# Kernel tuning notes

Measured on AMD Instinct MI355X. Metric: run time of the kernel, lower is better.

Reference implementation:

```python
import jax, jax.numpy as jnp
import numpy as np

TREE_DEPTH = 10
TOTAL = 2 ** (TREE_DEPTH + 1) - 1  # 2047 nodes per tree
G = 64                              # graphs per batch
N = G * TOTAL                       # 131008 nodes
E = 2 * N                           # 262016 directed edges
H = 256                             # h_dim
HALF = H // 2
L = 4                               # num_layers
LABELS = 32
OUT = 32
BN_EPS = 1e-5
LN_EPS = 1e-5


def setup_inputs() -> dict:
    key = jax.random.key(0)
    ks = jax.random.split(key, 16)
    x = jnp.stack([jax.random.randint(ks[0], (N,), 0, TOTAL),
                   jax.random.randint(ks[1], (N,), 0, LABELS)], axis=1)
    edge_src = jax.random.randint(ks[2], (E,), 0, N)
    edge_dst = jax.random.randint(ks[3], (E,), 0, N)
    edge_weight = jax.random.uniform(ks[4], (E,), dtype=jnp.float32)
    batch = jnp.arange(N, dtype=jnp.int64) // TOTAL          # node -> graph id
    root_index = jnp.arange(G, dtype=jnp.int64) * TOTAL      # one root per graph
    s = 0.02
    emb_node = jax.random.normal(ks[5], (TOTAL, HALF), dtype=jnp.float32) * s
    emb_label = jax.random.normal(ks[6], (LABELS, HALF), dtype=jnp.float32) * s
    w = 1.0 / np.sqrt(H)
    W1 = jax.random.normal(ks[7], (L, H, H), dtype=jnp.float32) * w
    b1 = jnp.zeros((L, H), dtype=jnp.float32)
    g1 = jnp.ones((L, H), dtype=jnp.float32)
    be1 = jnp.zeros((L, H), dtype=jnp.float32)
    W2 = jax.random.normal(ks[8], (L, H, H), dtype=jnp.float32) * w
    b2 = jnp.zeros((L, H), dtype=jnp.float32)
    g2 = jnp.ones((L, H), dtype=jnp.float32)
    be2 = jnp.zeros((L, H), dtype=jnp.float32)
    ln_g = jnp.ones((L, H), dtype=jnp.float32)
    ln_b = jnp.zeros((L, H), dtype=jnp.float32)
    Wout = jax.random.normal(ks[9], (OUT, H), dtype=jnp.float32) * w
    return {"x": x, "edge_src": edge_src, "edge_dst": edge_dst,
            "edge_weight": edge_weight, "batch": batch, "root_index": root_index,
            "emb_node": emb_node, "emb_label": emb_label,
            "W1": W1, "b1": b1, "g1": g1, "be1": be1,
            "W2": W2, "b2": b2, "g2": g2, "be2": be2,
            "ln_g": ln_g, "ln_b": ln_b, "Wout": Wout}


def _batchnorm(h, g, b):
    # BatchNorm1d, training-mode batch statistics over the node dim
    m = h.mean(axis=0)
    v = h.var(axis=0)
    return g * (h - m) * jax.lax.rsqrt(v + BN_EPS) + b


def _layernorm(h, g, b):
    m = h.mean(axis=-1, keepdims=True)
    v = h.var(axis=-1, keepdims=True)
    return g * (h - m) * jax.lax.rsqrt(v + LN_EPS) + b


def reference(x, edge_src, edge_dst, edge_weight, batch, root_index,
              emb_node, emb_label, W1, b1, g1, be1, W2, b2, g2, be2,
              ln_g, ln_b, Wout):
    # BiEmbedding_cat: concat of two h/2 embeddings
    h = jnp.concatenate([emb_node[x[:, 0]], emb_label[x[:, 1]]], axis=-1)  # [N,H]
    target_roots = root_index[batch]  # all-nodes->root targets for last layer
    for i in range(L):
        if i == L - 1:  # last_layer_fully_adjacent: every node sends to its root
            agg = jnp.zeros_like(h).at[target_roots].add(h)
        else:
            agg = jnp.zeros_like(h).at[edge_dst].add(h[edge_src] * edge_weight[:, None])
        m = h + agg  # GIN with eps=0: (1+eps)*x + sum_j w_ij x_j
        m = jax.nn.relu(_batchnorm(m @ W1[i].T + b1[i], g1[i], be1[i]))
        m = jax.nn.relu(_batchnorm(m @ W2[i].T + b2[i], g2[i], be2[i]))
        # use_activation: relu (idempotent after the MLP's trailing relu)
        h = h + m  # use_residual
        h = _layernorm(h, ln_g[i], ln_b[i])
    roots_x = h[root_index]  # [G,H] root readout
    return roots_x @ Wout.T  # [G,OUT], bias-free out layer
```

## Files before the change

### kernel.cpp

```cpp
#include <hip/hip_runtime.h>
#include <stdint.h>

#define NN 131008
#define NPAD 131072
#define EE 262016
#define HD 256
#define GG 64
#define TT 2047

typedef __attribute__((ext_vector_type(8))) short bfrag;
typedef __attribute__((ext_vector_type(4))) float f32x4;

__device__ __forceinline__ float bflo(unsigned u){ union{unsigned i; float f;} v; v.i = u<<16; return v.f; }
__device__ __forceinline__ float bfhi(unsigned u){ union{unsigned i; float f;} v; v.i = u & 0xffff0000u; return v.f; }
__device__ __forceinline__ unsigned short f2bf(float f){
  union{unsigned i; float fl;} v; v.fl = f; unsigned i = v.i;
  return (unsigned short)((i + 0x7fffu + ((i>>16)&1u)) >> 16);
}
__device__ __forceinline__ unsigned pack2(float a, float b){
  return (unsigned)f2bf(a) | ((unsigned)f2bf(b)<<16);
}
__device__ __forceinline__ void gload16(const void* g, void* s){
  __builtin_amdgcn_global_load_lds((__attribute__((address_space(1))) void*)g,
                                   (__attribute__((address_space(3))) void*)s, 16, 0, 0);
}

__device__ __forceinline__ short bnrelu1(short t, float a, float c){
  union{unsigned i; float f;} v; v.i = ((unsigned)(unsigned short)t) << 16;
  return (short)f2bf(fmaxf(a*v.f + c, 0.f));
}
__device__ __forceinline__ bfrag bn8(bfrag t, float4 a0, float4 a1, float4 c0, float4 c1){
  bfrag r;
  r[0]=bnrelu1(t[0],a0.x,c0.x); r[1]=bnrelu1(t[1],a0.y,c0.y);
  r[2]=bnrelu1(t[2],a0.z,c0.z); r[3]=bnrelu1(t[3],a0.w,c0.w);
  r[4]=bnrelu1(t[4],a1.x,c1.x); r[5]=bnrelu1(t[5],a1.y,c1.y);
  r[6]=bnrelu1(t[6],a1.z,c1.z); r[7]=bnrelu1(t[7],a1.w,c1.w);
  return r;
}

__device__ __forceinline__ void atomic_add_bf16x2(unsigned short* p, float a, float b){
#if __has_builtin(__builtin_amdgcn_global_atomic_fadd_v2bf16)
  typedef __attribute__((ext_vector_type(2))) short s16x2;
  s16x2 v; v.x = (short)f2bf(a); v.y = (short)f2bf(b);
  __builtin_amdgcn_global_atomic_fadd_v2bf16((__attribute__((address_space(1))) s16x2*)p, v);
#else
  unsigned* up = (unsigned*)p;
  unsigned old = *up, assumed;
  do {
    assumed = old;
    unsigned nv = pack2(bflo(assumed) + a, bfhi(assumed) + b);
    old = atomicCAS(up, assumed, nv);
  } while (old != assumed);
#endif
}

__global__ void k_prep(const float* __restrict__ W1, const float* __restrict__ W2,
                       unsigned short* __restrict__ wbf,
                       const int* __restrict__ x, const float* __restrict__ en,
                       const float* __restrict__ el, unsigned short* __restrict__ hbf,
                       const int* __restrict__ ed, int* __restrict__ deg){
  int b = blockIdx.x;
  if (b < 2048){
    int idx = b*256 + threadIdx.x;
    float v = (idx < 262144) ? W1[idx] : W2[idx - 262144];
    wbf[idx] = f2bf(v);
  } else if (b < 18432){
    size_t i8 = ((size_t)(b - 2048)*256 + threadIdx.x) << 3;
    int row = (int)(i8 >> 8); int k = (int)(i8 & 255);
    uint4 o;
    if (row < NN){
      const float* src = (k < 128) ? en + (size_t)x[2*row]*128 + k
                                   : el + (size_t)x[2*row+1]*128 + (k-128);
      float4 v0 = *(const float4*)src;
      float4 v1 = *(const float4*)(src + 4);
      o.x = pack2(v0.x, v0.y); o.y = pack2(v0.z, v0.w);
      o.z = pack2(v1.x, v1.y); o.w = pack2(v1.z, v1.w);
    } else { o.x = o.y = o.z = o.w = 0u; }
    *(uint4*)(hbf + i8) = o;
  } else {
    int e = (b - 18432)*256 + threadIdx.x;
    if (e < EE) atomicAdd(&deg[ed[e]], 1);
  }
}

__global__ void k_scan_block(const int* __restrict__ deg, int* __restrict__ start,
                             int* __restrict__ bsum){
  __shared__ int sh[256];
  int t = threadIdx.x;
  int i = blockIdx.x*256 + t;
  int v = deg[i];
  int val = v; sh[t] = val; __syncthreads();
  for (int off = 1; off < 256; off <<= 1){
    int add = (t >= off) ? sh[t-off] : 0;
    __syncthreads();
    val += add; sh[t] = val;
    __syncthreads();
  }
  start[i] = val - v;
  if (t == 255) bsum[blockIdx.x] = val;
}
__global__ void k_scan_top(int* __restrict__ bsum){
  __shared__ int sh[512];
  int t = threadIdx.x;
  int v = bsum[t];
  int val = v; sh[t] = val; __syncthreads();
  for (int off = 1; off < 512; off <<= 1){
    int add = (t >= off) ? sh[t-off] : 0;
    __syncthreads();
    val += add; sh[t] = val;
    __syncthreads();
  }
  bsum[t] = val - v;
}
__global__ void k_fill(const int* __restrict__ es, const int* __restrict__ ed,
                       const float* __restrict__ ew, const int* __restrict__ start,
                       const int* __restrict__ bsum,
                       int* __restrict__ cursor0, uint2* __restrict__ pairs){
  int e = blockIdx.x*256 + threadIdx.x;
  if (e < EE){
    int d = ed[e];
    int pos = start[d] + bsum[d >> 8] + atomicAdd(&cursor0[d], 1);
    uint2 p; p.x = (unsigned)es[e];
    union{float f; unsigned u;} w; w.f = ew[e];
    p.y = w.u;
    pairs[pos] = p;
  }
}

__global__ void k_gather(const int* __restrict__ deg, const int* __restrict__ start,
                         const int* __restrict__ bsum,
                         const uint2* __restrict__ pairs,
                         const unsigned short* __restrict__ hbf,
                         unsigned short* __restrict__ mbf){
  int half = threadIdx.x >> 5, lane32 = threadIdx.x & 31;
  int row = blockIdx.x*8 + half;
  size_t base = (size_t)row*HD + (lane32 << 3);
  uint4 o;
  if (row < NN){
    uint4 hv = *(const uint4*)(hbf + base);
    float a0 = bflo(hv.x), a1 = bfhi(hv.x), a2 = bflo(hv.y), a3 = bfhi(hv.y);
    float a4 = bflo(hv.z), a5 = bfhi(hv.z), a6 = bflo(hv.w), a7 = bfhi(hv.w);
    int d = deg[row], s = start[row] + bsum[row >> 8];
    for (int j = 0; j < d; ++j){
      uint2 pr = pairs[s + j];
      union{unsigned u; float f;} wg; wg.u = pr.y;
      uint4 sv = *(const uint4*)(hbf + (size_t)pr.x*HD + (lane32 << 3));
      a0 += bflo(sv.x)*wg.f; a1 += bfhi(sv.x)*wg.f;
      a2 += bflo(sv.y)*wg.f; a3 += bfhi(sv.y)*wg.f;
      a4 += bflo(sv.z)*wg.f; a5 += bfhi(sv.z)*wg.f;
      a6 += bflo(sv.w)*wg.f; a7 += bfhi(sv.w)*wg.f;
    }
    o.x = pack2(a0, a1); o.y = pack2(a2, a3);
    o.z = pack2(a4, a5); o.w = pack2(a6, a7);
  } else { o.x = o.y = o.z = o.w = 0u; }
  *(uint4*)(mbf + base) = o;
}

__global__ void k_rootsum(const unsigned short* __restrict__ hbf, unsigned short* __restrict__ m){
  int g = blockIdx.x >> 4, ch = blockIdx.x & 15;
  int col = threadIdx.x * 2;
  int nr = (ch == 15) ? 127 : 128;
  const unsigned short* p = hbf + ((size_t)g*TT + ch*128)*HD + col;
  float a = 0.f, b = 0.f;
  for (int r = 0; r < nr; ++r){
    unsigned u = *(const unsigned*)(p + (size_t)r*HD);
    a += bflo(u); b += bfhi(u);
  }
  atomic_add_bf16x2(m + (size_t)g*TT*HD + col, a, b);
}

__global__ __launch_bounds__(512) void k_gemm(const unsigned short* __restrict__ A,
                                              const unsigned short* __restrict__ B,
                                              unsigned short* __restrict__ C,
                                              float* __restrict__ gsum, float* __restrict__ gsq){
  __shared__ unsigned short As[128*64];
  __shared__ unsigned short Bs[256*64];
  __shared__ float rs[256];
  __shared__ float rq[256];
  const int tid = threadIdx.x, lane = tid & 63, w = tid >> 6;
  const int wr = w >> 2, wc = w & 3;
  const int mb = blockIdx.x;
  if (tid < 256){ rs[tid] = 0.f; rq[tid] = 0.f; }
  f32x4 acc[4][4];
  f32x4 zz = {0.f, 0.f, 0.f, 0.f};
#pragma unroll
  for (int a = 0; a < 4; ++a)
#pragma unroll
    for (int b = 0; b < 4; ++b) acc[a][b] = zz;

  for (int kt = 0; kt < 4; ++kt){
    __syncthreads();
#pragma unroll
    for (int it = 0; it < 2; ++it){
      int ci = it*512 + tid;
      int row = ci >> 3, cp = ci & 7;
      int cl = cp ^ (row & 7);
      gload16(A + ((size_t)mb*128 + row)*HD + kt*64 + cl*8, &As[ci*8]);
    }
#pragma unroll
    for (int it = 0; it < 4; ++it){
      int ci = it*512 + tid;
      int row = ci >> 3, cp = ci & 7;
      int cl = cp ^ (row & 7);
      gload16(B + (size_t)row*HD + kt*64 + cl*8, &Bs[ci*8]);
    }
    __syncthreads();
    bfrag af[4][2], bfv[4][2];
    {
      const int q = lane >> 4, r15 = lane & 15, r7 = lane & 7;
#pragma unroll
      for (int rt = 0; rt < 4; ++rt){
        int ra = wr*64 + rt*16 + r15;
        int rb = wc*64 + rt*16 + r15;
#pragma unroll
        for (int hf = 0; hf < 2; ++hf){
          af[rt][hf]  = *(const bfrag*)&As[ra*64 + (((q + 4*hf) ^ r7) << 3)];
          bfv[rt][hf] = *(const bfrag*)&Bs[rb*64 + (((q + 4*hf) ^ r7) << 3)];
        }
      }
    }
#pragma unroll
    for (int hf = 0; hf < 2; ++hf)
#pragma unroll
      for (int rt = 0; rt < 4; ++rt)
#pragma unroll
        for (int ct = 0; ct < 4; ++ct)
          acc[rt][ct] = __builtin_amdgcn_mfma_f32_16x16x32_bf16(af[rt][hf], bfv[ct][hf], acc[rt][ct], 0, 0, 0);
  }

  const int lr0 = wr*64 + (lane >> 4)*4;
  const int lc0 = wc*64 + (lane & 15);
  float cs[4] = {0.f,0.f,0.f,0.f}, cq[4] = {0.f,0.f,0.f,0.f};
#pragma unroll
  for (int rt = 0; rt < 4; ++rt){
#pragma unroll
    for (int ct = 0; ct < 4; ++ct){
#pragma unroll
      for (int i = 0; i < 4; ++i){
        size_t grow = (size_t)mb*128 + lr0 + rt*16 + i;
        float v = acc[rt][ct][i];
        C[grow*HD + lc0 + ct*16] = f2bf(v);
        if (grow < NN){ cs[ct] += v; cq[ct] += v*v; }
      }
    }
  }
#pragma unroll
  for (int ct = 0; ct < 4; ++ct){
    float s = cs[ct], q = cq[ct];
    s += __shfl_xor(s, 16); s += __shfl_xor(s, 32);
    q += __shfl_xor(q, 16); q += __shfl_xor(q, 32);
    if ((lane >> 4) == 0){
      atomicAdd(&rs[lc0 + ct*16], s);
      atomicAdd(&rq[lc0 + ct*16], q);
    }
  }
  __syncthreads();
  if (tid < 256){
    atomicAdd(&gsum[tid], rs[tid]);
    atomicAdd(&gsq[tid], rq[tid]);
  }
}

__global__ __launch_bounds__(512) void k_gemm2(const unsigned short* __restrict__ T,
                                               const float* __restrict__ sum1,
                                               const float* __restrict__ sq1,
                                               const float* __restrict__ g1v,
                                               const float* __restrict__ be1v,
                                               const unsigned short* __restrict__ B,
                                               unsigned short* __restrict__ C,
                                               float* __restrict__ gsum, float* __restrict__ gsq){
  __shared__ unsigned short As[128*64];
  __shared__ unsigned short Bs[256*64];
  __shared__ float rs[256];
  __shared__ float rq[256];
  __shared__ float acf[256];
  __shared__ float ccf[256];
  const int tid = threadIdx.x, lane = tid & 63, w = tid >> 6;
  const int wr = w >> 2, wc = w & 3;
  const int mb = blockIdx.x;
  if (tid < 256){
    rs[tid] = 0.f; rq[tid] = 0.f;
    const float inv_n = 1.f/(float)NN;
    float mean = sum1[tid] * inv_n;
    float var  = fmaxf(sq1[tid] * inv_n - mean*mean, 0.f);
    float aj   = g1v[tid] * rsqrtf(var + 1e-5f);
    acf[tid] = aj;
    ccf[tid] = be1v[tid] - aj*mean;
  }
  f32x4 acc[4][4];
  f32x4 zz = {0.f, 0.f, 0.f, 0.f};
#pragma unroll
  for (int a = 0; a < 4; ++a)
#pragma unroll
    for (int b = 0; b < 4; ++b) acc[a][b] = zz;

  for (int kt = 0; kt < 4; ++kt){
    __syncthreads();
#pragma unroll
    for (int it = 0; it < 2; ++it){
      int ci = it*512 + tid;
      int row = ci >> 3, cp = ci & 7;
      int cl = cp ^ (row & 7);
      gload16(T + ((size_t)mb*128 + row)*HD + kt*64 + cl*8, &As[ci*8]);
    }
#pragma unroll
    for (int it = 0; it < 4; ++it){
      int ci = it*512 + tid;
      int row = ci >> 3, cp = ci & 7;
      int cl = cp ^ (row & 7);
      gload16(B + (size_t)row*HD + kt*64 + cl*8, &Bs[ci*8]);
    }
    asm volatile("s_waitcnt vmcnt(4)" ::: "memory");
#pragma unroll
    for (int it = 0; it < 2; ++it){
      int ci = it*512 + tid;
      int row = ci >> 3, cp = ci & 7;
      int kb = (cp ^ (row & 7)) << 3;
      bfrag v = *(const bfrag*)&As[ci*8];
      float4 a0 = *(const float4*)&acf[kt*64 + kb];
      float4 a1 = *(const float4*)&acf[kt*64 + kb + 4];
      float4 c0 = *(const float4*)&ccf[kt*64 + kb];
      float4 c1 = *(const float4*)&ccf[kt*64 + kb + 4];
      *(bfrag*)&As[ci*8] = bn8(v, a0, a1, c0, c1);
    }
    __syncthreads();
    bfrag af[4][2], bfv[4][2];
    {
      const int q = lane >> 4, r15 = lane & 15, r7 = lane & 7;
#pragma unroll
      for (int rt = 0; rt < 4; ++rt){
        int ra = wr*64 + rt*16 + r15;
        int rb = wc*64 + rt*16 + r15;
#pragma unroll
        for (int hf = 0; hf < 2; ++hf){
          af[rt][hf]  = *(const bfrag*)&As[ra*64 + (((q + 4*hf) ^ r7) << 3)];
          bfv[rt][hf] = *(const bfrag*)&Bs[rb*64 + (((q + 4*hf) ^ r7) << 3)];
        }
      }
    }
#pragma unroll
    for (int hf = 0; hf < 2; ++hf)
#pragma unroll
      for (int rt = 0; rt < 4; ++rt)
#pragma unroll
        for (int ct = 0; ct < 4; ++ct)
          acc[rt][ct] = __builtin_amdgcn_mfma_f32_16x16x32_bf16(af[rt][hf], bfv[ct][hf], acc[rt][ct], 0, 0, 0);
  }

  const int lr0 = wr*64 + (lane >> 4)*4;
  const int lc0 = wc*64 + (lane & 15);
  float cs[4] = {0.f,0.f,0.f,0.f}, cq[4] = {0.f,0.f,0.f,0.f};
#pragma unroll
  for (int rt = 0; rt < 4; ++rt){
#pragma unroll
    for (int ct = 0; ct < 4; ++ct){
#pragma unroll
      for (int i = 0; i < 4; ++i){
        size_t grow = (size_t)mb*128 + lr0 + rt*16 + i;
        float v = acc[rt][ct][i];
        C[grow*HD + lc0 + ct*16] = f2bf(v);
        if (grow < NN){ cs[ct] += v; cq[ct] += v*v; }
      }
    }
  }
#pragma unroll
  for (int ct = 0; ct < 4; ++ct){
    float s = cs[ct], q = cq[ct];
    s += __shfl_xor(s, 16); s += __shfl_xor(s, 32);
    q += __shfl_xor(q, 16); q += __shfl_xor(q, 32);
    if ((lane >> 4) == 0){
      atomicAdd(&rs[lc0 + ct*16], s);
      atomicAdd(&rq[lc0 + ct*16], q);
    }
  }
  __syncthreads();
  if (tid < 256){
    atomicAdd(&gsum[tid], rs[tid]);
    atomicAdd(&gsq[tid], rq[tid]);
  }
}

__device__ __forceinline__ void coef4(float4 s4, float4 q4, float4 g4, float4 b4,
                                      float4& a, float4& c){
  const float inv_n = 1.f/(float)NN;
  float m0 = s4.x*inv_n, m1 = s4.y*inv_n, m2 = s4.z*inv_n, m3 = s4.w*inv_n;
  float i0 = rsqrtf(fmaxf(q4.x*inv_n - m0*m0, 0.f) + 1e-5f);
  float i1 = rsqrtf(fmaxf(q4.y*inv_n - m1*m1, 0.f) + 1e-5f);
  float i2 = rsqrtf(fmaxf(q4.z*inv_n - m2*m2, 0.f) + 1e-5f);
  float i3 = rsqrtf(fmaxf(q4.w*inv_n - m3*m3, 0.f) + 1e-5f);
  a.x = g4.x*i0; a.y = g4.y*i1; a.z = g4.z*i2; a.w = g4.w*i3;
  c.x = b4.x - a.x*m0; c.y = b4.y - a.y*m1; c.z = b4.z - a.z*m2; c.w = b4.w - a.w*m3;
}

__global__ void k_fuse(const unsigned short* t2,
                       const float* __restrict__ sum, const float* __restrict__ sq,
                       const float* __restrict__ g, const float* __restrict__ be,
                       const float* __restrict__ lg, const float* __restrict__ lb,
                       unsigned short* __restrict__ hbf, unsigned short* mbf,
                       int writem){
  int half = threadIdx.x >> 5, lane32 = threadIdx.x & 31;
  size_t row = (size_t)blockIdx.x*8 + half;
  int col = lane32 << 3;
  size_t base = row*HD + col;
  uint4 o;
  if (row < NN){
    float4 av0, cv0, av1, cv1;
    coef4(*(const float4*)(sum + col),     *(const float4*)(sq + col),
          *(const float4*)(g + col),       *(const float4*)(be + col),     av0, cv0);
    coef4(*(const float4*)(sum + col + 4), *(const float4*)(sq + col + 4),
          *(const float4*)(g + col + 4),   *(const float4*)(be + col + 4), av1, cv1);
    uint4 tv = *(const uint4*)(t2 + base);
    uint4 hv = *(const uint4*)(hbf + base);
    float r0 = bflo(hv.x) + fmaxf(av0.x*bflo(tv.x) + cv0.x, 0.f);
    float r1 = bfhi(hv.x) + fmaxf(av0.y*bfhi(tv.x) + cv0.y, 0.f);
    float r2 = bflo(hv.y) + fmaxf(av0.z*bflo(tv.y) + cv0.z, 0.f);
    float r3 = bfhi(hv.y) + fmaxf(av0.w*bfhi(tv.y) + cv0.w, 0.f);
    float r4 = bflo(hv.z) + fmaxf(av1.x*bflo(tv.z) + cv1.x, 0.f);
    float r5 = bfhi(hv.z) + fmaxf(av1.y*bfhi(tv.z) + cv1.y, 0.f);
    float r6 = bflo(hv.w) + fmaxf(av1.z*bflo(tv.w) + cv1.z, 0.f);
    float r7 = bfhi(hv.w) + fmaxf(av1.w*bfhi(tv.w) + cv1.w, 0.f);
    float s  = r0+r1+r2+r3+r4+r5+r6+r7;
    float qq = r0*r0+r1*r1+r2*r2+r3*r3+r4*r4+r5*r5+r6*r6+r7*r7;
#pragma unroll
    for (int d = 1; d < 32; d <<= 1){ s += __shfl_xor(s, d); qq += __shfl_xor(qq, d); }
    float mean = s * (1.f/256.f);
    float var  = fmaxf(qq * (1.f/256.f) - mean*mean, 0.f);
    float inv  = rsqrtf(var + 1e-5f);
    float4 gv0 = *(const float4*)(lg + col), gv1 = *(const float4*)(lg + col + 4);
    float4 bv0 = *(const float4*)(lb + col), bv1 = *(const float4*)(lb + col + 4);
    o.x = pack2(gv0.x*(r0 - mean)*inv + bv0.x, gv0.y*(r1 - mean)*inv + bv0.y);
    o.y = pack2(gv0.z*(r2 - mean)*inv + bv0.z, gv0.w*(r3 - mean)*inv + bv0.w);
    o.z = pack2(gv1.x*(r4 - mean)*inv + bv1.x, gv1.y*(r5 - mean)*inv + bv1.y);
    o.w = pack2(gv1.z*(r6 - mean)*inv + bv1.z, gv1.w*(r7 - mean)*inv + bv1.w);
  } else {
    o.x = o.y = o.z = o.w = 0u;
  }
  *(uint4*)(hbf + base) = o;
  if (writem) *(uint4*)(mbf + base) = o;
}

__global__ void k_readout(const unsigned short* __restrict__ hbf, const float* __restrict__ Wo,
                          float* __restrict__ out){
  int g = blockIdx.x;
  int w = threadIdx.x >> 6, lane = threadIdx.x & 63;
  uint2 hv = *(const uint2*)(hbf + (size_t)g*TT*HD + (lane<<2));
  float h0 = bflo(hv.x), h1 = bfhi(hv.x), h2 = bflo(hv.y), h3 = bfhi(hv.y);
#pragma unroll
  for (int oo = 0; oo < 8; ++oo){
    int o = w*8 + oo;
    float4 wv = *(const float4*)(Wo + (size_t)o*HD + (lane<<2));
    float p = h0*wv.x + h1*wv.y + h2*wv.z + h3*wv.w;
#pragma unroll
    for (int d = 1; d < 64; d <<= 1) p += __shfl_xor(p, d);
    if (lane == 0) out[g*32 + o] = p;
  }
}

extern "C" void kernel_launch(void* const* d_in, const int* in_sizes, int n_in,
                              void* d_out, int out_size, void* d_ws, size_t ws_size,
                              hipStream_t stream){
  const int*   x   = (const int*)d_in[0];
  const int*   es  = (const int*)d_in[1];
  const int*   ed  = (const int*)d_in[2];
  const float* ew  = (const float*)d_in[3];
  const float* en  = (const float*)d_in[6];
  const float* el  = (const float*)d_in[7];
  const float* W1  = (const float*)d_in[8];
  const float* g1  = (const float*)d_in[10];
  const float* be1 = (const float*)d_in[11];
  const float* W2  = (const float*)d_in[12];
  const float* g2  = (const float*)d_in[14];
  const float* be2 = (const float*)d_in[15];
  const float* lg  = (const float*)d_in[16];
  const float* lb  = (const float*)d_in[17];
  const float* Wo  = (const float*)d_in[18];

  char* ws = (char*)d_ws;
  unsigned short* hbf = (unsigned short*)ws;
  unsigned short* mbf = (unsigned short*)(ws + 67108864);
  unsigned short* t   = (unsigned short*)(ws + 134217728);
  unsigned short* wbf = (unsigned short*)(ws + 201326592);
  float* stats   = (float*)(ws + 202375168);
  int*   deg     = (int*)  (ws + 202391552);
  int*   cursor0 = (int*)  (ws + 202915840);
  int*   start   = (int*)  (ws + 203440128);
  int*   bsum    = (int*)  (ws + 203964416);
  uint2* pairs   = (uint2*)(ws + 203968512);

  hipMemsetAsync(stats, 0, 16384 + 524288 + 524288, stream);
  k_prep<<<19456, 256, 0, stream>>>(W1, W2, wbf, x, en, el, hbf, ed, deg);

  k_scan_block<<<512, 256, 0, stream>>>(deg, start, bsum);
  k_scan_top  <<<1,   512, 0, stream>>>(bsum);
  k_fill      <<<1024,256, 0, stream>>>(es, ed, ew, start, bsum, cursor0, pairs);

  for (int i = 0; i < 4; ++i){
    float* s1 = stats + (2*i)*512;
    float* s2 = stats + (2*i+1)*512;
    if (i < 3) k_gather <<<16384, 256, 0, stream>>>(deg, start, bsum, pairs, hbf, mbf);
    else       k_rootsum<<<1024,  128, 0, stream>>>(hbf, mbf);

    k_gemm <<<1024, 512, 0, stream>>>(mbf, wbf + i*65536, t, s1, s1 + 256);
    k_gemm2<<<1024, 512, 0, stream>>>(t, s1, s1 + 256, g1 + i*256, be1 + i*256,
                                      wbf + 262144 + i*65536, mbf, s2, s2 + 256);
    k_fuse <<<16384, 256, 0, stream>>>(mbf, s2, s2 + 256, g2 + i*256, be2 + i*256,
                                       lg + i*256, lb + i*256, hbf, mbf, (i == 2) ? 1 : 0);
  }

  k_readout<<<64, 256, 0, stream>>>(hbf, Wo, (float*)d_out);
  (void)in_sizes; (void)n_in; (void)out_size; (void)ws_size;
}
```

Measured before the change: 865.4 us.

## Make GEMMs persistent with resident weights and triple-buffered A pipeline

Both node-MLP GEMM kernels now share a templated body where each block loads the full 256x256 bf16 weight matrix into LDS once and then processes four 128-row tiles. A is streamed in 32-wide K slices through a three-slot buffer with async loads two stages ahead. The grid shrinks from 1024 to 256 blocks to amortise weight loading and BN-stat reduction. The cost is about 150KB of LDS per block, which limits occupancy to one block per CU and leaves 256 blocks on 256 CUs with no spare parallelism; the per-slice barriers also add synchronisation.

```diff
diff --git a/kernel.cpp b/kernel.cpp
--- a/kernel.cpp
+++ b/kernel.cpp
@@ -169,98 +169,153 @@
   atomic_add_bf16x2(m + (size_t)g*TT*HD + col, a, b);
 }
 
+template<bool TRANS>
+__device__ __forceinline__ void gemm_body(const unsigned short* __restrict__ A,
+                                          const unsigned short* __restrict__ B,
+                                          unsigned short* __restrict__ C,
+                                          float* __restrict__ gsum, float* __restrict__ gsq,
+                                          const float* __restrict__ sum1,
+                                          const float* __restrict__ sq1,
+                                          const float* __restrict__ g1v,
+                                          const float* __restrict__ be1v){
+  __shared__ unsigned short Bs[65536];
+  __shared__ unsigned short Ar[3*4096];
+  __shared__ float acf[256];
+  __shared__ float ccf[256];
+  const int tid = threadIdx.x, lane = tid & 63, w = tid >> 6;
+  const int wr = w >> 2, wc = w & 3;
+  const int b = blockIdx.x;
+  const int q = lane >> 4, r15 = lane & 15, r7 = lane & 7;
+  const int NTS = 32;
+
+  if (TRANS && tid < 256){
+    const float inv_n = 1.f/(float)NN;
+    float mean = sum1[tid] * inv_n;
+    float var  = fmaxf(sq1[tid] * inv_n - mean*mean, 0.f);
+    float aj   = g1v[tid] * rsqrtf(var + 1e-5f);
+    acf[tid] = aj;
+    ccf[tid] = be1v[tid] - aj*mean;
+  }
+
+#pragma unroll
+  for (int kt = 0; kt < 4; ++kt)
+#pragma unroll
+    for (int it = 0; it < 4; ++it){
+      int ci = it*512 + tid;
+      int row = ci >> 3, cp = ci & 7;
+      int cl = cp ^ (row & 7);
+      gload16(B + (size_t)row*HD + kt*64 + cl*8, &Bs[kt*16384 + ci*8]);
+    }
+  {
+    const int row = tid >> 2, cp = tid & 3;
+    gload16(A + ((size_t)(b*4)*128 + row)*HD + 0*32 + cp*8, &Ar[0*4096 + tid*8]);
+    gload16(A + ((size_t)(b*4)*128 + row)*HD + 1*32 + cp*8, &Ar[1*4096 + tid*8]);
+  }
+
+  f32x4 acc[4][4];
+  f32x4 zz = {0.f, 0.f, 0.f, 0.f};
+#pragma unroll
+  for (int a = 0; a < 4; ++a)
+#pragma unroll
+    for (int c = 0; c < 4; ++c) acc[a][c] = zz;
+  float cs[4] = {0.f,0.f,0.f,0.f}, cq[4] = {0.f,0.f,0.f,0.f};
+
+  for (int s = 0; s < NTS; ++s){
+    const int slot = s % 3;
+    if (s == NTS-1) asm volatile("s_waitcnt vmcnt(0)" ::: "memory");
+    else            asm volatile("s_waitcnt vmcnt(1)" ::: "memory");
+    asm volatile("s_waitcnt lgkmcnt(0)" ::: "memory");
+    __builtin_amdgcn_s_barrier();
+    __builtin_amdgcn_sched_barrier(0);
+
+    if (s + 2 < NTS){
+      const int c = s + 2;
+      const int tile2 = b*4 + (c >> 3), ks2 = c & 7;
+      const int row = tid >> 2, cp = tid & 3;
+      gload16(A + ((size_t)tile2*128 + row)*HD + ks2*32 + cp*8,
+              &Ar[(c % 3)*4096 + tid*8]);
+    }
+
+    if (TRANS){
+      const int ks = s & 7;
+      const int kb = ks*32 + (tid & 3)*8;
+      bfrag v = *(const bfrag*)&Ar[slot*4096 + tid*8];
+      float4 a0 = *(const float4*)&acf[kb];
+      float4 a1 = *(const float4*)&acf[kb + 4];
+      float4 c0 = *(const float4*)&ccf[kb];
+      float4 c1 = *(const float4*)&ccf[kb + 4];
+      *(bfrag*)&Ar[slot*4096 + tid*8] = bn8(v, a0, a1, c0, c1);
+      asm volatile("s_waitcnt lgkmcnt(0)" ::: "memory");
+      __builtin_amdgcn_s_barrier();
+      __builtin_amdgcn_sched_barrier(0);
+    }
+
+    const int kt64 = (s >> 1) & 3, hf = s & 1;
+    bfrag af[4], bf[4];
+#pragma unroll
+    for (int rt = 0; rt < 4; ++rt){
+      int ra = wr*64 + rt*16 + r15;
+      af[rt] = *(const bfrag*)&Ar[slot*4096 + ra*32 + (q << 3)];
+    }
+#pragma unroll
+    for (int ct = 0; ct < 4; ++ct){
+      int rb = wc*64 + ct*16 + r15;
+      bf[ct] = *(const bfrag*)&Bs[kt64*16384 + rb*64 + (((q + 4*hf) ^ r7) << 3)];
+    }
+#pragma unroll
+    for (int rt = 0; rt < 4; ++rt)
+#pragma unroll
+      for (int ct = 0; ct < 4; ++ct)
+        acc[rt][ct] = __builtin_amdgcn_mfma_f32_16x16x32_bf16(af[rt], bf[ct], acc[rt][ct], 0, 0, 0);
+
+    if ((s & 7) == 7){
+      const int tile = b*4 + (s >> 3);
+      const int lr0 = wr*64 + q*4;
+      const int lc0 = wc*64 + r15;
+#pragma unroll
+      for (int rt = 0; rt < 4; ++rt)
+#pragma unroll
+        for (int ct = 0; ct < 4; ++ct){
+#pragma unroll
+          for (int i = 0; i < 4; ++i){
+            size_t grow = (size_t)tile*128 + lr0 + rt*16 + i;
+            float v = acc[rt][ct][i];
+            C[grow*HD + lc0 + ct*16] = f2bf(v);
+            if (grow < NN){ cs[ct] += v; cq[ct] += v*v; }
+          }
+          acc[rt][ct] = zz;
+        }
+    }
+  }
+
+  __syncthreads();
+  float* st = (float*)Ar;
+  st[tid < 512 ? tid : 0] = 0.f;
+  __syncthreads();
+  const int lc0 = wc*64 + r15;
+#pragma unroll
+  for (int ct = 0; ct < 4; ++ct){
+    float s2 = cs[ct], q2 = cq[ct];
+    s2 += __shfl_xor(s2, 16); s2 += __shfl_xor(s2, 32);
+    q2 += __shfl_xor(q2, 16); q2 += __shfl_xor(q2, 32);
+    if (q == 0){
+      atomicAdd(&st[lc0 + ct*16], s2);
+      atomicAdd(&st[256 + lc0 + ct*16], q2);
+    }
+  }
+  __syncthreads();
+  if (tid < 256){
+    atomicAdd(&gsum[tid], st[tid]);
+    atomicAdd(&gsq[tid], st[256 + tid]);
+  }
+}
+
 __global__ __launch_bounds__(512) void k_gemm(const unsigned short* __restrict__ A,
                                               const unsigned short* __restrict__ B,
                                               unsigned short* __restrict__ C,
                                               float* __restrict__ gsum, float* __restrict__ gsq){
-  __shared__ unsigned short As[128*64];
-  __shared__ unsigned short Bs[256*64];
-  __shared__ float rs[256];
-  __shared__ float rq[256];
-  const int tid = threadIdx.x, lane = tid & 63, w = tid >> 6;
-  const int wr = w >> 2, wc = w & 3;
-  const int mb = blockIdx.x;
-  if (tid < 256){ rs[tid] = 0.f; rq[tid] = 0.f; }
-  f32x4 acc[4][4];
-  f32x4 zz = {0.f, 0.f, 0.f, 0.f};
-#pragma unroll
-  for (int a = 0; a < 4; ++a)
-#pragma unroll
-    for (int b = 0; b < 4; ++b) acc[a][b] = zz;
-
-  for (int kt = 0; kt < 4; ++kt){
-    __syncthreads();
-#pragma unroll
-    for (int it = 0; it < 2; ++it){
-      int ci = it*512 + tid;
-      int row = ci >> 3, cp = ci & 7;
-      int cl = cp ^ (row & 7);
-      gload16(A + ((size_t)mb*128 + row)*HD + kt*64 + cl*8, &As[ci*8]);
-    }
-#pragma unroll
-    for (int it = 0; it < 4; ++it){
-      int ci = it*512 + tid;
-      int row = ci >> 3, cp = ci & 7;
-      int cl = cp ^ (row & 7);
-      gload16(B + (size_t)row*HD + kt*64 + cl*8, &Bs[ci*8]);
-    }
-    __syncthreads();
-    bfrag af[4][2], bfv[4][2];
-    {
-      const int q = lane >> 4, r15 = lane & 15, r7 = lane & 7;
-#pragma unroll
-      for (int rt = 0; rt < 4; ++rt){
-        int ra = wr*64 + rt*16 + r15;
-        int rb = wc*64 + rt*16 + r15;
-#pragma unroll
-        for (int hf = 0; hf < 2; ++hf){
-          af[rt][hf]  = *(const bfrag*)&As[ra*64 + (((q + 4*hf) ^ r7) << 3)];
-          bfv[rt][hf] = *(const bfrag*)&Bs[rb*64 + (((q + 4*hf) ^ r7) << 3)];
-        }
-      }
-    }
-#pragma unroll
-    for (int hf = 0; hf < 2; ++hf)
-#pragma unroll
-      for (int rt = 0; rt < 4; ++rt)
-#pragma unroll
-        for (int ct = 0; ct < 4; ++ct)
-          acc[rt][ct] = __builtin_amdgcn_mfma_f32_16x16x32_bf16(af[rt][hf], bfv[ct][hf], acc[rt][ct], 0, 0, 0);
-  }
-
-  const int lr0 = wr*64 + (lane >> 4)*4;
-  const int lc0 = wc*64 + (lane & 15);
-  float cs[4] = {0.f,0.f,0.f,0.f}, cq[4] = {0.f,0.f,0.f,0.f};
-#pragma unroll
-  for (int rt = 0; rt < 4; ++rt){
-#pragma unroll
-    for (int ct = 0; ct < 4; ++ct){
-#pragma unroll
-      for (int i = 0; i < 4; ++i){
-        size_t grow = (size_t)mb*128 + lr0 + rt*16 + i;
-        float v = acc[rt][ct][i];
-        C[grow*HD + lc0 + ct*16] = f2bf(v);
-        if (grow < NN){ cs[ct] += v; cq[ct] += v*v; }
-      }
-    }
-  }
-#pragma unroll
-  for (int ct = 0; ct < 4; ++ct){
-    float s = cs[ct], q = cq[ct];
-    s += __shfl_xor(s, 16); s += __shfl_xor(s, 32);
-    q += __shfl_xor(q, 16); q += __shfl_xor(q, 32);
-    if ((lane >> 4) == 0){
-      atomicAdd(&rs[lc0 + ct*16], s);
-      atomicAdd(&rq[lc0 + ct*16], q);
-    }
-  }
-  __syncthreads();
-  if (tid < 256){
-    atomicAdd(&gsum[tid], rs[tid]);
-    atomicAdd(&gsq[tid], rq[tid]);
-  }
-}
-
+  gemm_body<false>(A, B, C, gsum, gsq, nullptr, nullptr, nullptr, nullptr);
+}
 __global__ __launch_bounds__(512) void k_gemm2(const unsigned short* __restrict__ T,
                                                const float* __restrict__ sum1,
                                                const float* __restrict__ sq1,
@@ -269,115 +324,7 @@
                                                const unsigned short* __restrict__ B,
                                                unsigned short* __restrict__ C,
                                                float* __restrict__ gsum, float* __restrict__ gsq){
-  __shared__ unsigned short As[128*64];
-  __shared__ unsigned short Bs[256*64];
-  __shared__ float rs[256];
-  __shared__ float rq[256];
-  __shared__ float acf[256];
-  __shared__ float ccf[256];
-  const int tid = threadIdx.x, lane = tid & 63, w = tid >> 6;
-  const int wr = w >> 2, wc = w & 3;
-  const int mb = blockIdx.x;
-  if (tid < 256){
-    rs[tid] = 0.f; rq[tid] = 0.f;
-    const float inv_n = 1.f/(float)NN;
-    float mean = sum1[tid] * inv_n;
-    float var  = fmaxf(sq1[tid] * inv_n - mean*mean, 0.f);
-    float aj   = g1v[tid] * rsqrtf(var + 1e-5f);
-    acf[tid] = aj;
-    ccf[tid] = be1v[tid] - aj*mean;
-  }
-  f32x4 acc[4][4];
-  f32x4 zz = {0.f, 0.f, 0.f, 0.f};
-#pragma unroll
-  for (int a = 0; a < 4; ++a)
-#pragma unroll
-    for (int b = 0; b < 4; ++b) acc[a][b] = zz;
-
-  for (int kt = 0; kt < 4; ++kt){
-    __syncthreads();
-#pragma unroll
-    for (int it = 0; it < 2; ++it){
-      int ci = it*512 + tid;
-      int row = ci >> 3, cp = ci & 7;
-      int cl = cp ^ (row & 7);
-      gload16(T + ((size_t)mb*128 + row)*HD + kt*64 + cl*8, &As[ci*8]);
-    }
-#pragma unroll
-    for (int it = 0; it < 4; ++it){
-      int ci = it*512 + tid;
-      int row = ci >> 3, cp = ci & 7;
-      int cl = cp ^ (row & 7);
-      gload16(B + (size_t)row*HD + kt*64 + cl*8, &Bs[ci*8]);
-    }
-    asm volatile("s_waitcnt vmcnt(4)" ::: "memory");
-#pragma unroll
-    for (int it = 0; it < 2; ++it){
-      int ci = it*512 + tid;
-      int row = ci >> 3, cp = ci & 7;
-      int kb = (cp ^ (row & 7)) << 3;
-      bfrag v = *(const bfrag*)&As[ci*8];
-      float4 a0 = *(const float4*)&acf[kt*64 + kb];
-      float4 a1 = *(const float4*)&acf[kt*64 + kb + 4];
-      float4 c0 = *(const float4*)&ccf[kt*64 + kb];
-      float4 c1 = *(const float4*)&ccf[kt*64 + kb + 4];
-      *(bfrag*)&As[ci*8] = bn8(v, a0, a1, c0, c1);
-    }
-    __syncthreads();
-    bfrag af[4][2], bfv[4][2];
-    {
-      const int q = lane >> 4, r15 = lane & 15, r7 = lane & 7;
-#pragma unroll
-      for (int rt = 0; rt < 4; ++rt){
-        int ra = wr*64 + rt*16 + r15;
-        int rb = wc*64 + rt*16 + r15;
-#pragma unroll
-        for (int hf = 0; hf < 2; ++hf){
-          af[rt][hf]  = *(const bfrag*)&As[ra*64 + (((q + 4*hf) ^ r7) << 3)];
-          bfv[rt][hf] = *(const bfrag*)&Bs[rb*64 + (((q + 4*hf) ^ r7) << 3)];
-        }
-      }
-    }
-#pragma unroll
-    for (int hf = 0; hf < 2; ++hf)
-#pragma unroll
-      for (int rt = 0; rt < 4; ++rt)
-#pragma unroll
-        for (int ct = 0; ct < 4; ++ct)
-          acc[rt][ct] = __builtin_amdgcn_mfma_f32_16x16x32_bf16(af[rt][hf], bfv[ct][hf], acc[rt][ct], 0, 0, 0);
-  }
-
-  const int lr0 = wr*64 + (lane >> 4)*4;
-  const int lc0 = wc*64 + (lane & 15);
-  float cs[4] = {0.f,0.f,0.f,0.f}, cq[4] = {0.f,0.f,0.f,0.f};
-#pragma unroll
-  for (int rt = 0; rt < 4; ++rt){
-#pragma unroll
-    for (int ct = 0; ct < 4; ++ct){
-#pragma unroll
-      for (int i = 0; i < 4; ++i){
-        size_t grow = (size_t)mb*128 + lr0 + rt*16 + i;
-        float v = acc[rt][ct][i];
-        C[grow*HD + lc0 + ct*16] = f2bf(v);
-        if (grow < NN){ cs[ct] += v; cq[ct] += v*v; }
-      }
-    }
-  }
-#pragma unroll
-  for (int ct = 0; ct < 4; ++ct){
-    float s = cs[ct], q = cq[ct];
-    s += __shfl_xor(s, 16); s += __shfl_xor(s, 32);
-    q += __shfl_xor(q, 16); q += __shfl_xor(q, 32);
-    if ((lane >> 4) == 0){
-      atomicAdd(&rs[lc0 + ct*16], s);
-      atomicAdd(&rq[lc0 + ct*16], q);
-    }
-  }
-  __syncthreads();
-  if (tid < 256){
-    atomicAdd(&gsum[tid], rs[tid]);
-    atomicAdd(&gsq[tid], rq[tid]);
-  }
+  gemm_body<true>(T, B, C, gsum, gsq, sum1, sq1, g1v, be1v);
 }
 
 __device__ __forceinline__ void coef4(float4 s4, float4 q4, float4 g4, float4 b4,
@@ -500,9 +447,9 @@
     if (i < 3) k_gather <<<16384, 256, 0, stream>>>(deg, start, bsum, pairs, hbf, mbf);
     else       k_rootsum<<<1024,  128, 0, stream>>>(hbf, mbf);
 
-    k_gemm <<<1024, 512, 0, stream>>>(mbf, wbf + i*65536, t, s1, s1 + 256);
-    k_gemm2<<<1024, 512, 0, stream>>>(t, s1, s1 + 256, g1 + i*256, be1 + i*256,
-                                      wbf + 262144 + i*65536, mbf, s2, s2 + 256);
+    k_gemm <<<256, 512, 0, stream>>>(mbf, wbf + i*65536, t, s1, s1 + 256);
+    k_gemm2<<<256, 512, 0, stream>>>(t, s1, s1 + 256, g1 + i*256, be1 + i*256,
+                                     wbf + 262144 + i*65536, mbf, s2, s2 + 256);
     k_fuse <<<16384, 256, 0, stream>>>(mbf, s2, s2 + 256, g2 + i*256, be2 + i*256,
                                        lg + i*256, lb + i*256, hbf, mbf, (i == 2) ? 1 : 0);
   }
```

New measurement: 807.9 us. 6.6% less time.
